# Kernel optimization log

Hardware: AMD Instinct MI355X
Metric: run time of the kernel (lower is better)

The kernel has to match this reference:

```python
import jax, jax.numpy as jnp
import numpy as np

N = 50000; E = 1600000; H = 128; R = 8; T = 2; P = 1000; M = 223


def setup_inputs() -> dict:
    key = jax.random.key(0)
    ks = jax.random.split(key, 16)
    s = 1.0 / np.sqrt(H).astype(np.float32)
    inp = {}
    inp['neigh_type_count'] = jax.random.uniform(ks[0], (N, 2), dtype=jnp.float32) * 5.0
    inp['norm'] = jax.random.uniform(ks[1], (E,), dtype=jnp.float32) + 0.1
    inp['special_cost'] = jax.random.uniform(ks[2], (N,), dtype=jnp.float32)
    inp['gt_map'] = jax.random.uniform(ks[3], (M, M), dtype=jnp.float32)
    inp['fc_w'] = jax.random.normal(ks[4], (2, H), dtype=jnp.float32) * (1.0 / np.sqrt(2.0))
    inp['fc_b'] = jnp.zeros((H,), jnp.float32)
    inp['w_nt'] = jax.random.normal(ks[5], (T, H, H), dtype=jnp.float32) * s
    inp['w_rel'] = jax.random.normal(ks[6], (R, H, H), dtype=jnp.float32) * s
    inp['fc2_w'] = jax.random.normal(ks[7], (H, 1), dtype=jnp.float32) * s
    inp['fc2_b'] = jnp.zeros((1,), jnp.float32)
    inp['fc3_w'] = jax.random.normal(ks[8], (H, 1), dtype=jnp.float32) * s
    inp['fc3_b'] = jnp.zeros((1,), jnp.float32)
    inp['fl3_w'] = jax.random.normal(ks[9], (H, P), dtype=jnp.float32) * s
    inp['fl3_b'] = jnp.zeros((P,), jnp.float32)
    inp['node_type'] = jax.random.randint(ks[10], (N,), 0, T, dtype=jnp.int32)
    inp['src'] = jax.random.randint(ks[11], (E,), 0, N, dtype=jnp.int32)
    inp['dst'] = jax.random.randint(ks[12], (E,), 0, N, dtype=jnp.int32)
    inp['etype'] = jax.random.randint(ks[13], (E,), 0, R, dtype=jnp.int32)
    return inp


def reference(neigh_type_count, norm, special_cost, gt_map, fc_w, fc_b, w_nt, w_rel,
              fc2_w, fc2_b, fc3_w, fc3_b, fl3_w, fl3_b, node_type, src, dst, etype):
    n = neigh_type_count.shape[0]
    # fc: [N,2] -> [N,H]
    h0 = neigh_type_count @ fc_w + fc_b
    # input RGCN layer: per-src-node-type transform, then per-edge-relation transform.
    # Compute node x type / node x relation products once, then gather per edge
    # (same math as per-edge bmm with gathered weights, far less traffic).
    h_nt_all = jnp.einsum('ni,tio->nto', h0, w_nt)                 # [N,T,H]
    h_nt = jnp.take_along_axis(h_nt_all, node_type[:, None, None].astype(jnp.int32), axis=1)[:, 0, :]  # [N,H]
    h_rel = jnp.einsum('ni,rio->nro', h_nt, w_rel)                 # [N,R,H]
    msg = h_rel[src, etype] * norm[:, None]                        # [E,H]
    h = jax.ops.segment_sum(msg, dst, num_segments=n)              # scatter-sum -> [N,H]
    h = jax.nn.relu(h)                                             # apply_func activation
    # fc2 + clamp(sigmoid)
    pred = jnp.clip(jax.nn.sigmoid(h @ fc2_w + fc2_b), 1e-7, 1e10) # [N,1]
    m = gt_map.shape[0]
    pm = pred[:m * m, 0].reshape(m, m)                             # pred node map [M,M]
    ce = -jnp.sum(gt_map * jnp.log2(pm))                           # min cross-entropy (single GT map)
    rs = jnp.sum(pm, axis=1)                                       # row sums [M]
    cs = jnp.sum(pm, axis=0)                                       # col sums [M]
    loss2 = jnp.sum(pm * (rs[:, None] - pm)) + jnp.sum(pm * (cs[None, :] - pm))
    sumone = jnp.sum((rs - 1.0) ** 2) + jnp.sum((cs - 1.0) ** 2)
    # fc_for_loss3 (sigmoid probs; summed so params get grads)
    prob3_sum = jnp.sum(jax.nn.sigmoid(h @ fl3_w + fl3_b))
    # OutputLayer: scatter-sum src pred_prob to dst, (sum-1)^2 * special_cost
    agg = jax.ops.segment_sum(pred[src, 0], dst, num_segments=n)
    out_cost = jnp.sum(((agg - 1.0) ** 2) * special_cost)
    # dgl.mean_nodes (single graph) + fc3
    gembed = jnp.mean(h, axis=0)
    pred_obj = (gembed @ fc3_w + fc3_b)[0]
    return jnp.stack([pred_obj, sumone, loss2, ce, out_cost, prob3_sum])
```

## Files before the change

kernel.cpp:

```cpp
#include <hip/hip_runtime.h>

#define H 128
#define RNUM 8
#define TNUM 2
#define PNUM 1000
#define MNUM 223
#define BNODES 64
#define NBUCK 782
#define BCAP 2304
#define EPB 8192
#define CPAD 16

typedef __attribute__((ext_vector_type(8))) short bf16x8;
typedef __attribute__((ext_vector_type(4))) float f32x4;

__device__ __forceinline__ float fsig(float z) {
    return 1.0f / (1.0f + __expf(-z));
}
__device__ __forceinline__ float fsig_fast(float z) {
    return __builtin_amdgcn_rcpf(1.0f + __expf(-z));
}

__device__ __forceinline__ float wave_reduce(float v) {
#pragma unroll
    for (int off = 32; off > 0; off >>= 1) v += __shfl_down(v, off, 64);
    return v;
}

__device__ __forceinline__ unsigned short f2bf(float f) {
    unsigned int u = __float_as_uint(f);
    u += 0x7fffu + ((u >> 16) & 1u);
    return (unsigned short)(u >> 16);
}

__global__ __launch_bounds__(1024) void partition_setup(
        const int* __restrict__ src, const int* __restrict__ dst,
        const int* __restrict__ etype, const float* __restrict__ norm,
        const int* __restrict__ node_type, const float* __restrict__ ntc,
        int* __restrict__ cursor,
        uint2* __restrict__ buck, int E, int NP,
        const float* __restrict__ fl3_w, const float* __restrict__ fl3_b,
        unsigned short* __restrict__ wt, float* __restrict__ biasws,
        const float* __restrict__ fc_w, const float* __restrict__ fc_b,
        const float* __restrict__ w_nt, const float* __restrict__ w_rel,
        unsigned short* __restrict__ CbT) {
    int blk = blockIdx.x;
    int tid = threadIdx.x;
    if (blk < NP) {
        __shared__ int lh[NBUCK];
        __shared__ int gb[NBUCK];
        for (int i = tid; i < NBUCK; i += 1024) lh[i] = 0;
        __syncthreads();
        int base = blk * EPB;
        int e0 = base + tid * 8;
        int s[8], d[8], r[8]; float nm[8];
        if (e0 + 8 <= E) {
            *(int4*)(s)      = ((const int4*)(src + e0))[0];
            *(int4*)(s + 4)  = ((const int4*)(src + e0))[1];
            *(int4*)(d)      = ((const int4*)(dst + e0))[0];
            *(int4*)(d + 4)  = ((const int4*)(dst + e0))[1];
            *(int4*)(r)      = ((const int4*)(etype + e0))[0];
            *(int4*)(r + 4)  = ((const int4*)(etype + e0))[1];
            *(float4*)(nm)     = ((const float4*)(norm + e0))[0];
            *(float4*)(nm + 4) = ((const float4*)(norm + e0))[1];
        } else {
#pragma unroll
            for (int c = 0; c < 8; ++c) {
                int e = e0 + c;
                bool ok = (e < E);
                s[c] = ok ? src[e] : 0;
                d[c] = ok ? dst[e] : 0;
                r[c] = ok ? etype[e] : 0;
                nm[c] = ok ? norm[e] : 0.0f;
            }
        }
        int t8[8]; float2 cc8[8];
#pragma unroll
        for (int c = 0; c < 8; ++c) {
            t8[c] = node_type[s[c]];
            cc8[c] = ((const float2*)ntc)[s[c]];
        }
        uint2 pl[8]; int bb[8]; int rk[8];
#pragma unroll
        for (int c = 0; c < 8; ++c) {
            bb[c] = -1;
            if (e0 + c < E) {
                unsigned f0 = __float2uint_rn(nm[c] * cc8[c].x * 128.0f);
                unsigned f1 = __float2uint_rn(nm[c] * cc8[c].y * 128.0f);
                unsigned f2 = __float2uint_rn(nm[c] * 512.0f);
                int b = d[c] >> 6;
                int local = d[c] & 63;
                pl[c].x = (unsigned)s[c] | ((unsigned)local << 18) | ((unsigned)r[c] << 24) | ((unsigned)t8[c] << 27);
                pl[c].y = f0 | (f1 << 10) | (f2 << 20);
                bb[c] = b;
                rk[c] = atomicAdd(&lh[b], 1);
            }
        }
        __syncthreads();
        for (int i = tid; i < NBUCK; i += 1024) {
            if (lh[i] > 0) {
                int g = atomicAdd(&cursor[i * CPAD], lh[i]);
                gb[i] = (g < 0) ? 0 : (g > BCAP ? BCAP : g);
            }
        }
        __syncthreads();
#pragma unroll
        for (int c = 0; c < 8; ++c) {
            if (bb[c] >= 0) {
                int pos = gb[bb[c]] + rk[c];
                if (pos < BCAP) buck[(size_t)bb[c] * BCAP + pos] = pl[c];
            }
        }
    } else if (blk < NP + 128) {
        int p = (blk - NP) * 8 + (tid >> 7);
        int k = tid & 127;
        float v = (p < PNUM) ? fl3_w[(size_t)k * PNUM + p] : 0.0f;
        wt[(size_t)p * H + k] = f2bf(v);
        if (k == 0) biasws[p] = (p < PNUM) ? fl3_b[p] : -1.0e4f;
    } else {
        __shared__ float G[8][3][H];
        int g = tid >> 7;
        int tr = (blk - NP - 128) * 8 + g;
        int t = tr >> 3, r = tr & 7;
        int i = tid & 127;
        float a0 = 0.f, a1 = 0.f, a2 = 0.f;
#pragma unroll 8
        for (int j = 0; j < H; ++j) {
            float w = w_nt[((size_t)t * H + j) * H + i];
            a0 += fc_w[j] * w;
            a1 += fc_w[H + j] * w;
            a2 += fc_b[j] * w;
        }
        G[g][0][i] = a0; G[g][1][i] = a1; G[g][2][i] = a2;
        __syncthreads();
        float c0 = 0.f, c1 = 0.f, c2 = 0.f;
#pragma unroll 8
        for (int k = 0; k < H; ++k) {
            float w = w_rel[((size_t)r * H + k) * H + i];
            c0 += G[g][0][k] * w;
            c1 += G[g][1][k] * w;
            c2 += G[g][2][k] * w;
        }
        CbT[i * 64 + tr * 3 + 0] = f2bf(c0);
        CbT[i * 64 + tr * 3 + 1] = f2bf(c1);
        CbT[i * 64 + tr * 3 + 2] = f2bf(c2);
        if (tr == 0) {
            uint4 z = make_uint4(0u, 0u, 0u, 0u);
            *(uint4*)(CbT + i * 64 + 48) = z;
            *(uint4*)(CbT + i * 64 + 56) = z;
        }
    }
}

__global__ __launch_bounds__(256) void bucket_node(
        const uint2* __restrict__ buck, const int* __restrict__ cursor,
        const unsigned short* __restrict__ CbT,
        const float* __restrict__ fc2_w, const float* __restrict__ fc2_b,
        unsigned short* __restrict__ hb, float* __restrict__ pred,
        float* __restrict__ gpart, int N) {
    __shared__ float S[64 * 68];
    __shared__ unsigned short Cb[128 * 72];
    __shared__ float gloc[128];
    unsigned long long* P = (unsigned long long*)S;
    int tid = threadIdx.x;
    int bkt = blockIdx.x;
    for (int i = tid; i < 2048; i += 256) S[i] = 0.0f;
    for (int g = tid; g < 1024; g += 256) {
        int row = g >> 3, c = g & 7;
        uint4 v = ((const uint4*)CbT)[g];
        *(uint4*)(Cb + row * 72 + c * 8) = v;
    }
    if (tid < 128) gloc[tid] = 0.0f;
    __syncthreads();

    int cnt = cursor[bkt * CPAD];
    if (cnt > BCAP) cnt = BCAP;
    if (cnt < 0) cnt = 0;
    const uint2* bp = buck + (size_t)bkt * BCAP;
    for (int base = 0; base < cnt; base += 1024) {
        uint2 pl[4]; int ii[4];
#pragma unroll
        for (int j = 0; j < 4; ++j) {
            ii[j] = base + j * 256 + tid;
            pl[j] = (ii[j] < cnt) ? bp[ii[j]] : make_uint2(0u, 0u);
        }
#pragma unroll
        for (int j = 0; j < 4; ++j) {
            if (ii[j] < cnt) {
                int local = (pl[j].x >> 18) & 63;
                int tr = ((pl[j].x >> 24) & 7) + (((pl[j].x >> 27) & 1) << 3);
                unsigned y = pl[j].y;
                unsigned long long pk = (unsigned long long)(y & 1023u)
                                      | ((unsigned long long)((y >> 10) & 1023u) << 21)
                                      | ((unsigned long long)(y >> 20) << 42);
                atomicAdd(&P[local * 16 + tr], pk);
            }
        }
    }
    __syncthreads();

    unsigned long long rpk[4];
#pragma unroll
    for (int u = 0; u < 4; ++u) rpk[u] = P[tid * 4 + u];
    __syncthreads();
#pragma unroll
    for (int u = 0; u < 4; ++u) {
        int idx = tid * 4 + u;
        int local = idx >> 4, tr = idx & 15;
        float* p = S + local * 68 + tr * 3;
        p[0] = (float)(unsigned)(rpk[u] & 0x1FFFFFull) * (1.0f / 128.0f);
        p[1] = (float)(unsigned)((rpk[u] >> 21) & 0x1FFFFFull) * (1.0f / 128.0f);
        p[2] = (float)(unsigned)(rpk[u] >> 42) * (1.0f / 512.0f);
    }
    for (int idx = tid; idx < 1024; idx += 256) {
        int row = idx >> 4, c = idx & 15;
        S[row * 68 + 48 + c] = 0.0f;
    }
    __syncthreads();

    int lane = tid & 63, w = tid >> 6;
    int lrow = lane & 15, quad = lane >> 4;

    bf16x8 a[2];
#pragma unroll
    for (int ks = 0; ks < 2; ++ks) {
        const float* sp = S + (w * 16 + lrow) * 68 + ks * 32 + quad * 8;
        float4 f0 = *(const float4*)sp;
        float4 f1 = *(const float4*)(sp + 4);
        bf16x8 t;
        t[0] = (short)f2bf(f0.x); t[1] = (short)f2bf(f0.y);
        t[2] = (short)f2bf(f0.z); t[3] = (short)f2bf(f0.w);
        t[4] = (short)f2bf(f1.x); t[5] = (short)f2bf(f1.y);
        t[6] = (short)f2bf(f1.z); t[7] = (short)f2bf(f1.w);
        a[ks] = t;
    }

    f32x4 acc[8];
#pragma unroll
    for (int tn = 0; tn < 8; ++tn) acc[tn] = (f32x4){0.f, 0.f, 0.f, 0.f};
#pragma unroll
    for (int ks = 0; ks < 2; ++ks) {
#pragma unroll
        for (int tn = 0; tn < 8; ++tn) {
            bf16x8 b = *(const bf16x8*)(Cb + (tn * 16 + lrow) * 72 + ks * 32 + quad * 8);
            acc[tn] = __builtin_amdgcn_mfma_f32_16x16x32_bf16(a[ks], b, acc[tn], 0, 0, 0);
        }
    }

#pragma unroll
    for (int tn = 0; tn < 8; ++tn)
#pragma unroll
        for (int r = 0; r < 4; ++r) acc[tn][r] = fmaxf(acc[tn][r], 0.f);

    int vbase = bkt * BNODES + w * 16 + quad * 4;
#pragma unroll
    for (int r = 0; r < 4; ++r) {
        unsigned short* hrow = hb + (size_t)(vbase + r) * H + lrow;
#pragma unroll
        for (int tn = 0; tn < 8; ++tn) hrow[tn * 16] = f2bf(acc[tn][r]);
    }
    float pd[4];
#pragma unroll
    for (int r = 0; r < 4; ++r) {
        float s = 0.f;
#pragma unroll
        for (int tn = 0; tn < 8; ++tn) s += acc[tn][r] * fc2_w[tn * 16 + lrow];
        pd[r] = s;
    }
#pragma unroll
    for (int mask = 1; mask < 16; mask <<= 1)
#pragma unroll
        for (int r = 0; r < 4; ++r) pd[r] += __shfl_xor(pd[r], mask, 64);
    if (lrow == 0) {
#pragma unroll
        for (int r = 0; r < 4; ++r) {
            int v = vbase + r;
            if (v < N) {
                float z = pd[r] + fc2_b[0];
                pred[v] = fminf(fmaxf(fsig(z), 1e-7f), 1e10f);
            }
        }
    }
    float csum[8];
#pragma unroll
    for (int tn = 0; tn < 8; ++tn)
        csum[tn] = acc[tn][0] + acc[tn][1] + acc[tn][2] + acc[tn][3];
#pragma unroll
    for (int mask = 16; mask < 64; mask <<= 1)
#pragma unroll
        for (int tn = 0; tn < 8; ++tn) csum[tn] += __shfl_xor(csum[tn], mask, 64);
    if (lane < 16) {
#pragma unroll
        for (int tn = 0; tn < 8; ++tn) atomicAdd(&gloc[tn * 16 + lrow], csum[tn]);
    }
    __syncthreads();
    if (tid < 128) gpart[(size_t)bkt * 128 + tid] = gloc[tid];
}

__global__ __launch_bounds__(256, 2) void mega_kernel(
        const unsigned short* __restrict__ hb, const unsigned short* __restrict__ wt,
        const float* __restrict__ biasws, float* __restrict__ psum, int nb128,
        const uint2* __restrict__ buck, const int* __restrict__ cursor,
        const float* __restrict__ pred, const float* __restrict__ sc,
        const float* __restrict__ gt, float* __restrict__ ocpart, int N,
        float* __restrict__ rs, float* __restrict__ cs,
        float* __restrict__ cepart, float* __restrict__ sqpart,
        const float* __restrict__ gpart, float* __restrict__ gsum, int nbuck) {
    __shared__ unsigned short Bsh[128 * 136];
    __shared__ float red[12];
    int blk = blockIdx.x;
    int tid = threadIdx.x;
    int P1 = nb128;
    int P2 = P1 + nbuck;
    int P3 = P2 + 2 * MNUM;

    if (blk < P1) {
        int n0 = blk * 128;
        int lane = tid & 63, wid = tid >> 6;
        int wy = wid >> 1, wx = wid & 1;
        int lrow = lane & 15, quad = lane >> 4;

        bf16x8 a[4][4];
#pragma unroll
        for (int tm = 0; tm < 4; ++tm) {
            const unsigned short* arow = hb + (size_t)(n0 + wy * 64 + tm * 16 + lrow) * H + quad * 8;
#pragma unroll
            for (int ks = 0; ks < 4; ++ks)
                a[tm][ks] = *(const bf16x8*)(arow + ks * 32);
        }

        float lsum = 0.f;
        for (int pt = 0; pt < 8; ++pt) {
            __syncthreads();
            {
                int c = tid & 15;
                int r0 = tid >> 4;
#pragma unroll
                for (int it = 0; it < 8; ++it) {
                    int row = r0 + it * 16;
                    uint4 bv = *(const uint4*)(wt + (size_t)(pt * 128 + row) * H + c * 8);
                    *(uint4*)(Bsh + row * 136 + c * 8) = bv;
                }
            }
            __syncthreads();

            f32x4 acc[4][4];
#pragma unroll
            for (int tm = 0; tm < 4; ++tm)
#pragma unroll
                for (int tn = 0; tn < 4; ++tn)
                    acc[tm][tn] = (f32x4){0.f, 0.f, 0.f, 0.f};

            const unsigned short* Bbase = Bsh + (wx * 64 + lrow) * 136 + quad * 8;
#pragma unroll
            for (int ks = 0; ks < 4; ++ks) {
                bf16x8 b[4];
#pragma unroll
                for (int tn = 0; tn < 4; ++tn)
                    b[tn] = *(const bf16x8*)(Bbase + tn * 16 * 136 + ks * 32);
#pragma unroll
                for (int tm = 0; tm < 4; ++tm)
#pragma unroll
                    for (int tn = 0; tn < 4; ++tn)
                        acc[tm][tn] = __builtin_amdgcn_mfma_f32_16x16x32_bf16(a[tm][ks], b[tn], acc[tm][tn], 0, 0, 0);
            }

#pragma unroll
            for (int tn = 0; tn < 4; ++tn) {
                float bv = biasws[pt * 128 + wx * 64 + tn * 16 + lrow];
#pragma unroll
                for (int tm = 0; tm < 4; ++tm) {
#pragma unroll
                    for (int r = 0; r < 4; ++r)
                        lsum += fsig_fast(acc[tm][tn][r] + bv);
                }
            }
        }
        lsum = wave_reduce(lsum);
        if (lane == 0) red[wid] = lsum;
        __syncthreads();
        if (tid == 0)
            psum[blk] = red[0] + red[1] + red[2] + red[3];
    } else if (blk < P2) {
        int bkt = blk - P1;
        float* agg = (float*)Bsh;
        if (tid < BNODES) agg[tid] = 0.0f;
        __syncthreads();
        int cnt = cursor[bkt * CPAD];
        if (cnt > BCAP) cnt = BCAP;
        if (cnt < 0) cnt = 0;
        const uint2* bp = buck + (size_t)bkt * BCAP;
        for (int base = 0; base < cnt; base += 2048) {
            unsigned x[8]; float pv[8]; int ii[8];
#pragma unroll
            for (int j = 0; j < 8; ++j) {
                ii[j] = base + j * 256 + tid;
                x[j] = (ii[j] < cnt) ? bp[ii[j]].x : 0u;
            }
#pragma unroll
            for (int j = 0; j < 8; ++j)
                pv[j] = (ii[j] < cnt) ? pred[x[j] & 0x3FFFF] : 0.f;
#pragma unroll
            for (int j = 0; j < 8; ++j)
                if (ii[j] < cnt) atomicAdd(&agg[(x[j] >> 18) & 63], pv[j]);
        }
        __syncthreads();
        if (tid < 64) {
            float v = 0.f;
            int node = bkt * BNODES + tid;
            if (node < N) {
                float d = agg[tid] - 1.0f;
                v = d * d * sc[node];
            }
            v = wave_reduce(v);
            if (tid == 0) ocpart[bkt] = v;
        }
    } else if (blk < P3) {
        int rc = blk - P2;
        if (rc < MNUM) {
            float p = 0.f, ce = 0.f, sq = 0.f;
            if (tid < MNUM) {
                p = pred[rc * MNUM + tid];
                ce = -gt[rc * MNUM + tid] * __log2f(p);
                sq = p * p;
            }
            p = wave_reduce(p);
            ce = wave_reduce(ce);
            sq = wave_reduce(sq);
            int wid = tid >> 6;
            if ((tid & 63) == 0) { red[wid] = p; red[4 + wid] = ce; red[8 + wid] = sq; }
            __syncthreads();
            if (tid == 0) {
                rs[rc] = red[0] + red[1] + red[2] + red[3];
                cepart[rc] = red[4] + red[5] + red[6] + red[7];
                sqpart[rc] = red[8] + red[9] + red[10] + red[11];
            }
        } else {
            int j = rc - MNUM;
            float p = 0.f;
            if (tid < MNUM) p = pred[tid * MNUM + j];
            p = wave_reduce(p);
            if ((tid & 63) == 0) red[tid >> 6] = p;
            __syncthreads();
            if (tid == 0) cs[j] = red[0] + red[1] + red[2] + red[3];
        }
    } else {
        int dim = blk - P3;
        float s = 0.f;
        for (int b = tid; b < nbuck; b += 256) s += gpart[(size_t)b * 128 + dim];
        s = wave_reduce(s);
        if ((tid & 63) == 0) red[tid >> 6] = s;
        __syncthreads();
        if (tid == 0) gsum[dim] = red[0] + red[1] + red[2] + red[3];
    }
}

__global__ __launch_bounds__(1024) void tail_kernel(
        const float* __restrict__ rs, const float* __restrict__ cs,
        const float* __restrict__ cepart, const float* __restrict__ sqpart,
        const float* __restrict__ psum, int npsum,
        const float* __restrict__ ocpart, int nbuck,
        const float* __restrict__ gsum, const float* __restrict__ fc3_w,
        const float* __restrict__ fc3_b, const float* __restrict__ fl3_b,
        float* __restrict__ out, int N, int padrows) {
    __shared__ float red[16];
    int tid = threadIdx.x;
    int wid = tid >> 6, lane = tid & 63;
    float v = 0.f;
    if (tid < MNUM) {
        float a = rs[tid] - 1.0f, b = cs[tid] - 1.0f;
        v = a * a + b * b;
    }
    v = wave_reduce(v);
    if (lane == 0) red[wid] = v;
    __syncthreads();
    if (tid == 0) { float s = 0.f; for (int i = 0; i < 16; ++i) s += red[i]; out[1] = s; }
    __syncthreads();
    float ce = (tid < MNUM) ? cepart[tid] : 0.f;
    ce = wave_reduce(ce);
    if (lane == 0) red[wid] = ce;
    __syncthreads();
    if (tid == 0) { float s = 0.f; for (int i = 0; i < 16; ++i) s += red[i]; out[3] = s; }
    __syncthreads();
    float l2 = 0.f;
    if (tid < MNUM)
        l2 = rs[tid] * rs[tid] + cs[tid] * cs[tid] - 2.0f * sqpart[tid];
    l2 = wave_reduce(l2);
    if (lane == 0) red[wid] = l2;
    __syncthreads();
    if (tid == 0) { float s = 0.f; for (int i = 0; i < 16; ++i) s += red[i]; out[2] = s; }
    __syncthreads();
    float ps = 0.f;
    for (int i = tid; i < npsum; i += 1024) ps += psum[i];
    float ss = 0.f;
    for (int p = tid; p < PNUM; p += 1024) ss += fsig_fast(fl3_b[p]);
    float comb = ps - (float)padrows * ss;
    comb = wave_reduce(comb);
    if (lane == 0) red[wid] = comb;
    __syncthreads();
    if (tid == 0) { float s = 0.f; for (int i = 0; i < 16; ++i) s += red[i]; out[5] = s; }
    __syncthreads();
    float oc = 0.f;
    for (int b = tid; b < nbuck; b += 1024) oc += ocpart[b];
    oc = wave_reduce(oc);
    if (lane == 0) red[wid] = oc;
    __syncthreads();
    if (tid == 0) { float s = 0.f; for (int i = 0; i < 16; ++i) s += red[i]; out[4] = s; }
    __syncthreads();
    float pv = 0.f;
    if (tid < 128) pv = gsum[tid] * (1.0f / (float)N) * fc3_w[tid];
    pv = wave_reduce(pv);
    if (lane == 0) red[wid] = pv;
    __syncthreads();
    if (tid == 0) { float s = 0.f; for (int i = 0; i < 16; ++i) s += red[i]; out[0] = s + fc3_b[0]; }
}

extern "C" void kernel_launch(void* const* d_in, const int* in_sizes, int n_in,
                              void* d_out, int out_size, void* d_ws, size_t ws_size,
                              hipStream_t stream) {
    const float* ntc   = (const float*)d_in[0];
    const float* norm  = (const float*)d_in[1];
    const float* sc    = (const float*)d_in[2];
    const float* gt    = (const float*)d_in[3];
    const float* fc_w  = (const float*)d_in[4];
    const float* fc_b  = (const float*)d_in[5];
    const float* w_nt  = (const float*)d_in[6];
    const float* w_rel = (const float*)d_in[7];
    const float* fc2_w = (const float*)d_in[8];
    const float* fc2_b = (const float*)d_in[9];
    const float* fc3_w = (const float*)d_in[10];
    const float* fc3_b = (const float*)d_in[11];
    const float* fl3_w = (const float*)d_in[12];
    const float* fl3_b = (const float*)d_in[13];
    const int* node_type = (const int*)d_in[14];
    const int* src   = (const int*)d_in[15];
    const int* dst   = (const int*)d_in[16];
    const int* etype = (const int*)d_in[17];
    int N = in_sizes[2];
    int E = in_sizes[1];
    int nb128 = (N + 127) / 128;
    int padN  = nb128 * 128;
    int nbuck = padN / BNODES;
    int npsum = nb128;
    int NP = (E + EPB - 1) / EPB;

    float* ws   = (float*)d_ws;
    unsigned short* wt = (unsigned short*)ws;
    float* biasws = ws + 65536;
    float* gsum = ws + 66560;
    float* rs   = ws + 66688;
    float* cs   = ws + 66944;
    int*  cursor = (int*)(ws + 67200);
    float* psum = ws + 79744;
    float* cepart = ws + 80768;
    float* sqpart = ws + 81024;
    float* ocpart = ws + 81280;
    unsigned short* CbT = (unsigned short*)(ws + 82304);
    float* gpart  = ws + 86400;
    float* pred = ws + 186496;
    unsigned short* hb = (unsigned short*)(ws + 236496);
    uint2* buck = (uint2*)(ws + 3439568);
    float* out  = (float*)d_out;

    hipMemsetAsync(cursor, 0, NBUCK * CPAD * sizeof(int), stream);

    partition_setup<<<NP + 130, 1024, 0, stream>>>(src, dst, etype, norm, node_type, ntc,
                                                   cursor, buck, E, NP,
                                                   fl3_w, fl3_b, wt, biasws,
                                                   fc_w, fc_b, w_nt, w_rel, CbT);
    bucket_node<<<nbuck, 256, 0, stream>>>(buck, cursor, CbT, fc2_w, fc2_b,
                                           hb, pred, gpart, N);
    int megablocks = nb128 + nbuck + 2 * MNUM + 128;
    mega_kernel<<<megablocks, 256, 0, stream>>>(hb, wt, biasws, psum, nb128,
                                                buck, cursor, pred, sc, gt, ocpart, N,
                                                rs, cs, cepart, sqpart, gpart, gsum, nbuck);
    tail_kernel<<<1, 1024, 0, stream>>>(rs, cs, cepart, sqpart, psum, npsum, ocpart, nbuck,
                                        gsum, fc3_w, fc3_b, fl3_b, out, N, padN - N);
}
```

Baseline: 191.2 us.

## Fuse fl3 sigmoid-sum GEMM into bucket_node, drop global h buffer

Moves the h @ fl3_w sigmoid-sum GEMM out of mega_kernel and into bucket_node. Each 64-node block keeps its bf16 h tile in shared memory and streams the 1000-column weight matrix in 64-row chunks. This removes the global hb write and read-back and shortens mega_kernel. In exchange, each block now loads the whole fl3 weight matrix for only 64 rows instead of 128. The GEMM also runs with less reuse per block and more barriers, which makes bucket_node longer.

```diff
diff --git a/kernel.cpp b/kernel.cpp
--- a/kernel.cpp
+++ b/kernel.cpp
@@ -156,14 +156,21 @@
         const uint2* __restrict__ buck, const int* __restrict__ cursor,
         const unsigned short* __restrict__ CbT,
         const float* __restrict__ fc2_w, const float* __restrict__ fc2_b,
-        unsigned short* __restrict__ hb, float* __restrict__ pred,
-        float* __restrict__ gpart, int N) {
+        const unsigned short* __restrict__ wt, const float* __restrict__ biasws,
+        float* __restrict__ pred, float* __restrict__ gpart,
+        float* __restrict__ psum, int N) {
     __shared__ float S[64 * 68];
     __shared__ unsigned short Cb[128 * 72];
     __shared__ float gloc[128];
+    __shared__ float red[4];
     unsigned long long* P = (unsigned long long*)S;
+    unsigned short* hsh = (unsigned short*)S;
+    unsigned short* Bsh = Cb;
     int tid = threadIdx.x;
     int bkt = blockIdx.x;
+    int lane = tid & 63, w = tid >> 6;
+    int lrow = lane & 15, quad = lane >> 4;
+
     for (int i = tid; i < 2048; i += 256) S[i] = 0.0f;
     for (int g = tid; g < 1024; g += 256) {
         int row = g >> 3, c = g & 7;
@@ -217,9 +224,6 @@
         S[row * 68 + 48 + c] = 0.0f;
     }
     __syncthreads();
-
-    int lane = tid & 63, w = tid >> 6;
-    int lrow = lane & 15, quad = lane >> 4;
 
     bf16x8 a[2];
 #pragma unroll
@@ -234,6 +238,7 @@
         t[6] = (short)f2bf(f1.z); t[7] = (short)f2bf(f1.w);
         a[ks] = t;
     }
+    __syncthreads();
 
     f32x4 acc[8];
 #pragma unroll
@@ -246,19 +251,18 @@
             acc[tn] = __builtin_amdgcn_mfma_f32_16x16x32_bf16(a[ks], b, acc[tn], 0, 0, 0);
         }
     }
-
 #pragma unroll
     for (int tn = 0; tn < 8; ++tn)
 #pragma unroll
         for (int r = 0; r < 4; ++r) acc[tn][r] = fmaxf(acc[tn][r], 0.f);
 
+#pragma unroll
+    for (int r = 0; r < 4; ++r) {
+        unsigned short* hrow = hsh + (w * 16 + quad * 4 + r) * 136 + lrow;
+#pragma unroll
+        for (int tn = 0; tn < 8; ++tn) hrow[tn * 16] = f2bf(acc[tn][r]);
+    }
     int vbase = bkt * BNODES + w * 16 + quad * 4;
-#pragma unroll
-    for (int r = 0; r < 4; ++r) {
-        unsigned short* hrow = hb + (size_t)(vbase + r) * H + lrow;
-#pragma unroll
-        for (int tn = 0; tn < 8; ++tn) hrow[tn * 16] = f2bf(acc[tn][r]);
-    }
     float pd[4];
 #pragma unroll
     for (int r = 0; r < 4; ++r) {
@@ -295,96 +299,74 @@
     }
     __syncthreads();
     if (tid < 128) gpart[(size_t)bkt * 128 + tid] = gloc[tid];
-}
-
-__global__ __launch_bounds__(256, 2) void mega_kernel(
-        const unsigned short* __restrict__ hb, const unsigned short* __restrict__ wt,
-        const float* __restrict__ biasws, float* __restrict__ psum, int nb128,
+
+    bf16x8 a2[4];
+#pragma unroll
+    for (int ks = 0; ks < 4; ++ks)
+        a2[ks] = *(const bf16x8*)(hsh + (w * 16 + lrow) * 136 + ks * 32 + quad * 8);
+
+    float lsum = 0.f;
+    for (int st = 0; st < 16; ++st) {
+        uint4 v[4];
+        {
+            int row = tid >> 2, cq = tid & 3;
+            const uint4* sp4 = (const uint4*)(wt + (size_t)(st * 64 + row) * H);
+#pragma unroll
+            for (int i = 0; i < 4; ++i) v[i] = sp4[cq * 4 + i];
+        }
+        __syncthreads();
+        {
+            int row = tid >> 2, cq = tid & 3;
+#pragma unroll
+            for (int i = 0; i < 4; ++i)
+                *(uint4*)(Bsh + row * 136 + (cq * 4 + i) * 8) = v[i];
+        }
+        __syncthreads();
+
+        f32x4 acc2[4];
+#pragma unroll
+        for (int tn = 0; tn < 4; ++tn) acc2[tn] = (f32x4){0.f, 0.f, 0.f, 0.f};
+#pragma unroll
+        for (int ks = 0; ks < 4; ++ks) {
+            bf16x8 b[4];
+#pragma unroll
+            for (int tn = 0; tn < 4; ++tn)
+                b[tn] = *(const bf16x8*)(Bsh + (tn * 16 + lrow) * 136 + ks * 32 + quad * 8);
+#pragma unroll
+            for (int tn = 0; tn < 4; ++tn)
+                acc2[tn] = __builtin_amdgcn_mfma_f32_16x16x32_bf16(a2[ks], b[tn], acc2[tn], 0, 0, 0);
+        }
+#pragma unroll
+        for (int tn = 0; tn < 4; ++tn) {
+            float bv = biasws[st * 64 + tn * 16 + lrow];
+#pragma unroll
+            for (int r = 0; r < 4; ++r)
+                lsum += fsig_fast(acc2[tn][r] + bv);
+        }
+    }
+    lsum = wave_reduce(lsum);
+    if (lane == 0) red[w] = lsum;
+    __syncthreads();
+    if (tid == 0) psum[bkt] = red[0] + red[1] + red[2] + red[3];
+}
+
+__global__ __launch_bounds__(256) void mega_kernel(
         const uint2* __restrict__ buck, const int* __restrict__ cursor,
         const float* __restrict__ pred, const float* __restrict__ sc,
         const float* __restrict__ gt, float* __restrict__ ocpart, int N,
         float* __restrict__ rs, float* __restrict__ cs,
         float* __restrict__ cepart, float* __restrict__ sqpart,
         const float* __restrict__ gpart, float* __restrict__ gsum, int nbuck) {
-    __shared__ unsigned short Bsh[128 * 136];
+    __shared__ float aggl[BNODES];
     __shared__ float red[12];
     int blk = blockIdx.x;
     int tid = threadIdx.x;
-    int P1 = nb128;
-    int P2 = P1 + nbuck;
-    int P3 = P2 + 2 * MNUM;
+    int P1 = nbuck;
+    int P2 = P1 + 2 * MNUM;
 
     if (blk < P1) {
-        int n0 = blk * 128;
-        int lane = tid & 63, wid = tid >> 6;
-        int wy = wid >> 1, wx = wid & 1;
-        int lrow = lane & 15, quad = lane >> 4;
-
-        bf16x8 a[4][4];
-#pragma unroll
-        for (int tm = 0; tm < 4; ++tm) {
-            const unsigned short* arow = hb + (size_t)(n0 + wy * 64 + tm * 16 + lrow) * H + quad * 8;
-#pragma unroll
-            for (int ks = 0; ks < 4; ++ks)
-                a[tm][ks] = *(const bf16x8*)(arow + ks * 32);
-        }
-
-        float lsum = 0.f;
-        for (int pt = 0; pt < 8; ++pt) {
-            __syncthreads();
-            {
-                int c = tid & 15;
-                int r0 = tid >> 4;
-#pragma unroll
-                for (int it = 0; it < 8; ++it) {
-                    int row = r0 + it * 16;
-                    uint4 bv = *(const uint4*)(wt + (size_t)(pt * 128 + row) * H + c * 8);
-                    *(uint4*)(Bsh + row * 136 + c * 8) = bv;
-                }
-            }
-            __syncthreads();
-
-            f32x4 acc[4][4];
-#pragma unroll
-            for (int tm = 0; tm < 4; ++tm)
-#pragma unroll
-                for (int tn = 0; tn < 4; ++tn)
-                    acc[tm][tn] = (f32x4){0.f, 0.f, 0.f, 0.f};
-
-            const unsigned short* Bbase = Bsh + (wx * 64 + lrow) * 136 + quad * 8;
-#pragma unroll
-            for (int ks = 0; ks < 4; ++ks) {
-                bf16x8 b[4];
-#pragma unroll
-                for (int tn = 0; tn < 4; ++tn)
-                    b[tn] = *(const bf16x8*)(Bbase + tn * 16 * 136 + ks * 32);
-#pragma unroll
-                for (int tm = 0; tm < 4; ++tm)
-#pragma unroll
-                    for (int tn = 0; tn < 4; ++tn)
-                        acc[tm][tn] = __builtin_amdgcn_mfma_f32_16x16x32_bf16(a[tm][ks], b[tn], acc[tm][tn], 0, 0, 0);
-            }
-
-#pragma unroll
-            for (int tn = 0; tn < 4; ++tn) {
-                float bv = biasws[pt * 128 + wx * 64 + tn * 16 + lrow];
-#pragma unroll
-                for (int tm = 0; tm < 4; ++tm) {
-#pragma unroll
-                    for (int r = 0; r < 4; ++r)
-                        lsum += fsig_fast(acc[tm][tn][r] + bv);
-                }
-            }
-        }
-        lsum = wave_reduce(lsum);
-        if (lane == 0) red[wid] = lsum;
-        __syncthreads();
-        if (tid == 0)
-            psum[blk] = red[0] + red[1] + red[2] + red[3];
-    } else if (blk < P2) {
-        int bkt = blk - P1;
-        float* agg = (float*)Bsh;
-        if (tid < BNODES) agg[tid] = 0.0f;
+        int bkt = blk;
+        if (tid < BNODES) aggl[tid] = 0.0f;
         __syncthreads();
         int cnt = cursor[bkt * CPAD];
         if (cnt > BCAP) cnt = BCAP;
@@ -402,21 +384,21 @@
                 pv[j] = (ii[j] < cnt) ? pred[x[j] & 0x3FFFF] : 0.f;
 #pragma unroll
             for (int j = 0; j < 8; ++j)
-                if (ii[j] < cnt) atomicAdd(&agg[(x[j] >> 18) & 63], pv[j]);
+                if (ii[j] < cnt) atomicAdd(&aggl[(x[j] >> 18) & 63], pv[j]);
         }
         __syncthreads();
         if (tid < 64) {
             float v = 0.f;
             int node = bkt * BNODES + tid;
             if (node < N) {
-                float d = agg[tid] - 1.0f;
+                float d = aggl[tid] - 1.0f;
                 v = d * d * sc[node];
             }
             v = wave_reduce(v);
             if (tid == 0) ocpart[bkt] = v;
         }
-    } else if (blk < P3) {
-        int rc = blk - P2;
+    } else if (blk < P2) {
+        int rc = blk - P1;
         if (rc < MNUM) {
             float p = 0.f, ce = 0.f, sq = 0.f;
             if (tid < MNUM) {
@@ -445,7 +427,7 @@
             if (tid == 0) cs[j] = red[0] + red[1] + red[2] + red[3];
         }
     } else {
-        int dim = blk - P3;
+        int dim = blk - P2;
         float s = 0.f;
         for (int b = tid; b < nbuck; b += 256) s += gpart[(size_t)b * 128 + dim];
         s = wave_reduce(s);
@@ -541,7 +523,6 @@
     int nb128 = (N + 127) / 128;
     int padN  = nb128 * 128;
     int nbuck = padN / BNODES;
-    int npsum = nb128;
     int NP = (E + EPB - 1) / EPB;
 
     float* ws   = (float*)d_ws;
@@ -558,8 +539,7 @@
     unsigned short* CbT = (unsigned short*)(ws + 82304);
     float* gpart  = ws + 86400;
     float* pred = ws + 186496;
-    unsigned short* hb = (unsigned short*)(ws + 236496);
-    uint2* buck = (uint2*)(ws + 3439568);
+    uint2* buck = (uint2*)(ws + 236544);
     float* out  = (float*)d_out;
 
     hipMemsetAsync(cursor, 0, NBUCK * CPAD * sizeof(int), stream);
@@ -569,11 +549,10 @@
                                                    fl3_w, fl3_b, wt, biasws,
                                                    fc_w, fc_b, w_nt, w_rel, CbT);
     bucket_node<<<nbuck, 256, 0, stream>>>(buck, cursor, CbT, fc2_w, fc2_b,
-                                           hb, pred, gpart, N);
-    int megablocks = nb128 + nbuck + 2 * MNUM + 128;
-    mega_kernel<<<megablocks, 256, 0, stream>>>(hb, wt, biasws, psum, nb128,
-                                                buck, cursor, pred, sc, gt, ocpart, N,
+                                           wt, biasws, pred, gpart, psum, N);
+    int megablocks = nbuck + 2 * MNUM + 128;
+    mega_kernel<<<megablocks, 256, 0, stream>>>(buck, cursor, pred, sc, gt, ocpart, N,
                                                 rs, cs, cepart, sqpart, gpart, gsum, nbuck);
-    tail_kernel<<<1, 1024, 0, stream>>>(rs, cs, cepart, sqpart, psum, npsum, ocpart, nbuck,
+    tail_kernel<<<1, 1024, 0, stream>>>(rs, cs, cepart, sqpart, psum, nbuck, ocpart, nbuck,
                                         gsum, fc3_w, fc3_b, fl3_b, out, N, padN - N);
 }
```

Result: slower. 244.4 us (+27.9%).
